# Performance work log

Measured on AMD Instinct MI355X. Metric: run time of the kernel, lower is better.

Reference implementation:

```python
import jax, jax.numpy as jnp
import numpy as np

EPS = 1e-5
SLOPE = 0.2

def _leaky(x):
    return jnp.where(x >= 0, x, SLOPE * x)

def _bn(x, g, b, axes):
    # batch-norm in training mode: biased stats over `axes`, per remaining channel dim
    mu = jnp.mean(x, axis=axes, keepdims=True)
    var = jnp.var(x, axis=axes, keepdims=True)
    shape = [1] * x.ndim
    shape[2 if x.ndim == 5 else 1] = -1
    return (x - mu) * jax.lax.rsqrt(var + EPS) * g.reshape(shape) + b.reshape(shape)

def setup_inputs() -> dict:
    key = jax.random.key(0)
    ks = jax.random.split(key, 6)
    T, B, C, H, W, D = 17, 16, 512, 16, 16, 256
    return {
        "cond": jax.random.normal(ks[0], (B, D), jnp.float32),
        "xbar": jax.random.normal(ks[1], (T, B, C, H, W), jnp.float32),
        "lin_w": jax.random.normal(ks[2], (D, D), jnp.float32) * 0.05,
        "lin_b": jnp.zeros((D,), jnp.float32),
        "bn_s_g": jnp.ones((D,), jnp.float32),
        "bn_s_b": jnp.zeros((D,), jnp.float32),
        "conv1_w": jax.random.normal(ks[3], (C, C), jnp.float32) * 0.05,
        "bn1_g": jnp.ones((C,), jnp.float32),
        "bn1_b": jnp.zeros((C,), jnp.float32),
        "conv2_w": jax.random.normal(ks[4], (C, C + D), jnp.float32) * 0.05,
        "bn2_g": jnp.ones((C,), jnp.float32),
        "bn2_b": jnp.zeros((C,), jnp.float32),
        "conv3_w": jax.random.normal(ks[5], (1, C, 2, 2), jnp.float32) * 0.05,
    }

def reference(cond, xbar, lin_w, lin_b, bn_s_g, bn_s_b, conv1_w, bn1_g, bn1_b, conv2_w, bn2_g, bn2_b, conv3_w):
    # sent_map: Linear -> BatchNorm1d (over batch) -> LeakyReLU
    sent = cond @ lin_w.T + lin_b                       # [B, D]
    sent = _leaky(_bn(sent, bn_s_g, bn_s_b, axes=(0,)))

    motions = xbar[1:] - xbar[:-1]                      # [F, B, C, H, W]
    F, B, C, H, W = motions.shape

    # motion_map: 1x1 conv -> BN (per-frame stats, matching the python loop) -> LeakyReLU
    h = jnp.einsum('fbchw,oc->fbohw', motions, conv1_w)
    h = _leaky(_bn(h, bn1_g, bn1_b, axes=(1, 3, 4)))

    # broadcast sentence vector over space (replaces per-pixel python loop)
    sent_dupe = jnp.broadcast_to(sent[None, :, :, None, None], (F, B, sent.shape[1], H, W))
    ms = jnp.concatenate([h, sent_dupe], axis=2)        # [F, B, C+D, H, W]

    # predictor: 1x1 conv -> BN (per-frame) -> LeakyReLU -> 2x2 stride-2 conv
    h2 = jnp.einsum('fbchw,oc->fbohw', ms, conv2_w)
    h2 = _leaky(_bn(h2, bn2_g, bn2_b, axes=(1, 3, 4)))

    h2f = h2.reshape(F * B, C, H, W)
    out = jax.lax.conv_general_dilated(
        h2f, conv3_w, window_strides=(2, 2), padding='VALID',
        dimension_numbers=('NCHW', 'OIHW', 'NCHW'))     # [F*B, 1, H/2, W/2]
    return out.reshape(F, B, -1)                        # matches view(B,-1) per frame + stack
```

## Files before the change

### kernel.cpp

```cpp
#include <hip/hip_runtime.h>
#include <hip/hip_bf16.h>

#define EPS 1e-5f
#define SLOPE 0.2f

#define NF 16
#define NBATCH 16
#define NC 512
#define NHW 256
#define ND 256
#define K2 768
#define MF 4096
#define FRAME_ELEMS ((size_t)MF * NC)

typedef __attribute__((ext_vector_type(8))) short short8;
typedef __attribute__((ext_vector_type(4))) float float4v;

__device__ __forceinline__ float lrelu(float v) { return v >= 0.f ? v : SLOPE * v; }
__device__ __forceinline__ float b2f(ushort u) { union { float f; uint i; } x; x.i = ((uint)u) << 16; return x.f; }
__device__ __forceinline__ ushort f2b(float f) {
  uint i = __float_as_uint(f);
  return (ushort)((i + 0x7FFFu + ((i >> 16) & 1u)) >> 16);
}
__device__ __forceinline__ void gl16(const ushort* g, ushort* l) {
  __builtin_amdgcn_global_load_lds(
      (const __attribute__((address_space(1))) unsigned int*)g,
      (__attribute__((address_space(3))) unsigned int*)l, 16, 0, 0);
}

__global__ __launch_bounds__(256) void k_sent(
    const float* __restrict__ cond, const float* __restrict__ lin_w,
    const float* __restrict__ lin_b, const float* __restrict__ gam,
    const float* __restrict__ bet, float* __restrict__ sent) {
  int d = threadIdx.x;
  float acc[NBATCH];
  float bias = lin_b[d];
#pragma unroll
  for (int b = 0; b < NBATCH; ++b) acc[b] = bias;
  for (int k = 0; k < ND; ++k) {
    float w = lin_w[d * ND + k];
#pragma unroll
    for (int b = 0; b < NBATCH; ++b) acc[b] = fmaf(cond[b * ND + k], w, acc[b]);
  }
  float mu = 0.f;
#pragma unroll
  for (int b = 0; b < NBATCH; ++b) mu += acc[b];
  mu *= (1.f / NBATCH);
  float var = 0.f;
#pragma unroll
  for (int b = 0; b < NBATCH; ++b) { float t = acc[b] - mu; var = fmaf(t, t, var); }
  var *= (1.f / NBATCH);
  float sc = rsqrtf(var + EPS) * gam[d];
  float sh = bet[d] - mu * sc;
#pragma unroll
  for (int b = 0; b < NBATCH; ++b) sent[b * ND + d] = lrelu(fmaf(acc[b], sc, sh));
}

__global__ __launch_bounds__(256) void k_bias2(
    const float* __restrict__ sent, const float* __restrict__ w2,
    float* __restrict__ bias2) {
  int o = blockIdx.x * 256 + threadIdx.x;
  float acc[NBATCH];
#pragma unroll
  for (int b = 0; b < NBATCH; ++b) acc[b] = 0.f;
  for (int d = 0; d < ND; ++d) {
    float w = w2[(size_t)o * K2 + NC + d];
#pragma unroll
    for (int b = 0; b < NBATCH; ++b) acc[b] = fmaf(sent[b * ND + d], w, acc[b]);
  }
#pragma unroll
  for (int b = 0; b < NBATCH; ++b) bias2[b * NC + o] = acc[b];
}

__global__ __launch_bounds__(256) void k_wcvt(
    const float* __restrict__ w1, const float* __restrict__ w2,
    ushort* __restrict__ w1b, ushort* __restrict__ w2b) {
  int i = blockIdx.x * 256 + threadIdx.x;
  w1b[i] = f2b(w1[i]);
  int o = i >> 9, c = i & 511;
  w2b[i] = f2b(w2[(size_t)o * K2 + c]);
}

__global__ __launch_bounds__(256) void k_mot(
    const float* __restrict__ xbar, ushort* __restrict__ mot, int f0, int nb) {
  __shared__ float T[64][65];
  int b = blockIdx.y;
  int hw0 = (blockIdx.x & 3) * 64;
  int c0 = (blockIdx.x >> 2) * 64;
  int t = threadIdx.x;
  int w = t >> 6, l = t & 63;
  int fs = blockIdx.z * 4;
  int fe = fs + 4 < nb ? fs + 4 : nb;

  const float* xp = xbar + ((size_t)(f0 + fs) * NBATCH + b) * (NC * NHW) + hw0 + l;
  float prev[16];
#pragma unroll
  for (int k = 0; k < 16; ++k) prev[k] = xp[(size_t)(c0 + 4 * k + w) * NHW];

  for (int fr = fs; fr < fe; ++fr) {
    const float* xc = xbar + ((size_t)(f0 + fr + 1) * NBATCH + b) * (NC * NHW) + hw0 + l;
    float cur[16];
#pragma unroll
    for (int k = 0; k < 16; ++k) cur[k] = xc[(size_t)(c0 + 4 * k + w) * NHW];
#pragma unroll
    for (int k = 0; k < 16; ++k) T[4 * k + w][l] = cur[k] - prev[k];
    __syncthreads();
    ushort* mp = mot + ((size_t)fr * MF + b * NHW + hw0) * NC + c0;
#pragma unroll
    for (int k = 0; k < 16; ++k) mp[(size_t)(4 * k + w) * NC + l] = f2b(T[l][4 * k + w]);
    __syncthreads();
#pragma unroll
    for (int k = 0; k < 16; ++k) prev[k] = cur[k];
  }
}

template <int BIAS>
__global__ __launch_bounds__(256) void k_gemm(
    const ushort* __restrict__ A, const ushort* __restrict__ W,
    const float* __restrict__ bias2, ushort* __restrict__ H,
    float2* __restrict__ part) {
  __shared__ ushort lds[2][8192];
  int t = threadIdx.x;
  int w = t >> 6, l = t & 63;
  int g = blockIdx.z;
  int m0 = blockIdx.x * 128;
  int n0 = blockIdx.y * 128;
  int wr = w >> 1, wc = w & 1;

  const ushort* Ag = A + ((size_t)g * MF + m0) * NC;
  const ushort* Wg = W + (size_t)n0 * NC;

  float4v acc[4][4];
#pragma unroll
  for (int i = 0; i < 4; ++i)
#pragma unroll
    for (int j = 0; j < 4; ++j) acc[i][j] = (float4v)0.f;

  int s1 = (w * 2 + 0) * 64 + l;
  int s2 = (w * 2 + 1) * 64 + l;
  size_t ga1 = (size_t)(s1 >> 2) * NC + (s1 & 3) * 8;
  size_t ga2 = (size_t)(s2 >> 2) * NC + (s2 & 3) * 8;

#define STAGE(buf, c0)                                  \
  do {                                                  \
    gl16(Ag + ga1 + (c0), &lds[buf][s1 * 8]);           \
    gl16(Ag + ga2 + (c0), &lds[buf][s2 * 8]);           \
    gl16(Wg + ga1 + (c0), &lds[buf][4096 + s1 * 8]);    \
    gl16(Wg + ga2 + (c0), &lds[buf][4096 + s2 * 8]);    \
  } while (0)

  STAGE(0, 0);
  asm volatile("s_waitcnt vmcnt(0)" ::: "memory");
  __syncthreads();

  for (int kt = 0; kt < 16; ++kt) {
    int cur = kt & 1;
    if (kt < 15) STAGE(cur ^ 1, (kt + 1) * 32);
    short8 af[4], bfr[4];
#pragma unroll
    for (int i = 0; i < 4; ++i)
      af[i] = *(const short8*)&lds[cur][(wr * 64 + i * 16 + (l & 15)) * 32 + (l >> 4) * 8];
#pragma unroll
    for (int j = 0; j < 4; ++j)
      bfr[j] = *(const short8*)&lds[cur][4096 + (wc * 64 + j * 16 + (l & 15)) * 32 + (l >> 4) * 8];
#pragma unroll
    for (int i = 0; i < 4; ++i)
#pragma unroll
      for (int j = 0; j < 4; ++j)
        acc[i][j] = __builtin_amdgcn_mfma_f32_16x16x32_bf16(af[i], bfr[j], acc[i][j], 0, 0, 0);
    if (kt < 15) {
      asm volatile("s_waitcnt vmcnt(0)" ::: "memory");
      __syncthreads();
    }
  }
#undef STAGE
  __syncthreads();

  float bz[4];
#pragma unroll
  for (int fn = 0; fn < 4; ++fn)
    bz[fn] = BIAS ? bias2[(m0 >> 8) * NC + n0 + wc * 64 + fn * 16 + (l & 15)] : 0.f;

  float sv[4], qv[4];
#pragma unroll
  for (int fn = 0; fn < 4; ++fn) {
    float s = 0.f, q = 0.f;
#pragma unroll
    for (int fm = 0; fm < 4; ++fm)
#pragma unroll
      for (int j = 0; j < 4; ++j) {
        float v = acc[fm][fn][j] + bz[fn];
        acc[fm][fn][j] = v;
        s += v;
        q = fmaf(v, v, q);
      }
    s += __shfl_xor(s, 16); s += __shfl_xor(s, 32);
    q += __shfl_xor(q, 16); q += __shfl_xor(q, 32);
    sv[fn] = s; qv[fn] = q;
  }
  if (l < 16) {
    int mb = blockIdx.x * 2 + wr;
    float2* pp = part + ((size_t)g * 64 + mb) * NC + n0 + wc * 64 + l;
#pragma unroll
    for (int fn = 0; fn < 4; ++fn) pp[fn * 16] = make_float2(sv[fn], qv[fn]);
  }

  ushort* ep = &lds[0][w * 1088];
  ushort* Hg = H + ((size_t)g * MF + m0 + wr * 64) * NC + n0 + wc * 64;
#pragma unroll
  for (int fm = 0; fm < 4; ++fm) {
#pragma unroll
    for (int fn = 0; fn < 4; ++fn)
#pragma unroll
      for (int j = 0; j < 4; ++j)
        ep[((l >> 4) * 4 + j) * 68 + fn * 16 + (l & 15)] = f2b(acc[fm][fn][j]);
#pragma unroll
    for (int h = 0; h < 2; ++h) {
      int r = h * 8 + (l >> 3), sl = l & 7;
      short8 v = *(const short8*)&ep[r * 68 + sl * 8];
      *(short8*)&Hg[(size_t)(fm * 16 + r) * NC + sl * 8] = v;
    }
  }
}

__global__ __launch_bounds__(256) void k_stats2(
    const float2* __restrict__ part, const float* __restrict__ gam,
    const float* __restrict__ bet, float2* __restrict__ st) {
  int bi = blockIdx.x;
  int g = bi >> 1;
  int o = (bi & 1) * 256 + threadIdx.x;
  float s = 0.f, q = 0.f;
#pragma unroll
  for (int mb = 0; mb < 64; ++mb) {
    float2 v = part[((size_t)g * 64 + mb) * NC + o];
    s += v.x;
    q += v.y;
  }
  float mu = s * (1.f / 4096.f);
  float var = q * (1.f / 4096.f) - mu * mu;
  float sc = rsqrtf(var + EPS) * gam[o];
  st[g * NC + o] = make_float2(sc, bet[o] - mu * sc);
}

__global__ __launch_bounds__(256) void k_act(
    const ushort* __restrict__ h1, const float2* __restrict__ st,
    ushort* __restrict__ a2) {
  int g = blockIdx.z;
  size_t i0 = ((size_t)blockIdx.x * 256 + threadIdx.x) * 8;
  int o0 = (int)(i0 & 511);
  const ushort* src = h1 + (size_t)g * FRAME_ELEMS + i0;
  ushort* dst = a2 + (size_t)g * FRAME_ELEMS + i0;
  short8 v = *(const short8*)src;
  short8 r;
#pragma unroll
  for (int e = 0; e < 8; ++e) {
    float2 ss = st[g * NC + o0 + e];
    float x = fmaf(b2f((ushort)v[e]), ss.x, ss.y);
    r[e] = (short)f2b(lrelu(x));
  }
  *(short8*)dst = r;
}

__global__ __launch_bounds__(256) void k_conv3(
    const ushort* __restrict__ h2, const float2* __restrict__ st2,
    const float* __restrict__ w3, float* __restrict__ out, int f0) {
  int g = blockIdx.z;
  int b = blockIdx.x;
  int t = threadIdx.x;
  int oi = t >> 2;
  int cs = t & 3;
  int y = oi >> 3, x = oi & 7;
  const ushort* base = h2 + ((size_t)g * MF + b * NHW) * NC;
  int m00 = (2 * y) * 16 + 2 * x;
  float acc = 0.f;
  for (int c8 = cs * 128; c8 < cs * 128 + 128; c8 += 8) {
    short8 v0 = *(const short8*)&base[(size_t)(m00 + 0) * NC + c8];
    short8 v1 = *(const short8*)&base[(size_t)(m00 + 1) * NC + c8];
    short8 v2 = *(const short8*)&base[(size_t)(m00 + 16) * NC + c8];
    short8 v3 = *(const short8*)&base[(size_t)(m00 + 17) * NC + c8];
#pragma unroll
    for (int e = 0; e < 8; ++e) {
      float2 ss = st2[g * NC + c8 + e];
      float4 wv = ((const float4*)w3)[c8 + e];
      acc = fmaf(lrelu(fmaf(b2f((ushort)v0[e]), ss.x, ss.y)), wv.x, acc);
      acc = fmaf(lrelu(fmaf(b2f((ushort)v1[e]), ss.x, ss.y)), wv.y, acc);
      acc = fmaf(lrelu(fmaf(b2f((ushort)v2[e]), ss.x, ss.y)), wv.z, acc);
      acc = fmaf(lrelu(fmaf(b2f((ushort)v3[e]), ss.x, ss.y)), wv.w, acc);
    }
  }
  acc += __shfl_xor(acc, 1);
  acc += __shfl_xor(acc, 2);
  if (cs == 0) out[((size_t)(f0 + g) * NBATCH + b) * 64 + oi] = acc;
}

extern "C" void kernel_launch(void* const* d_in, const int* in_sizes, int n_in,
                              void* d_out, int out_size, void* d_ws, size_t ws_size,
                              hipStream_t stream) {
  const float* cond = (const float*)d_in[0];
  const float* xbar = (const float*)d_in[1];
  const float* lin_w = (const float*)d_in[2];
  const float* lin_b = (const float*)d_in[3];
  const float* bnsg = (const float*)d_in[4];
  const float* bnsb = (const float*)d_in[5];
  const float* w1 = (const float*)d_in[6];
  const float* bn1g = (const float*)d_in[7];
  const float* bn1b = (const float*)d_in[8];
  const float* w2 = (const float*)d_in[9];
  const float* bn2g = (const float*)d_in[10];
  const float* bn2b = (const float*)d_in[11];
  const float* w3 = (const float*)d_in[12];
  float* out = (float*)d_out;

  char* p = (char*)d_ws;
  float* sent = (float*)p;    p += ((NBATCH * ND * 4 + 255) & ~255);
  float* bias2 = (float*)p;   p += ((NBATCH * NC * 4 + 255) & ~255);
  float2* st1 = (float2*)p;   p += ((NF * NC * 8 + 255) & ~255);
  float2* st2 = (float2*)p;   p += ((NF * NC * 8 + 255) & ~255);
  float2* part = (float2*)p;  p += (((size_t)NF * 64 * NC * 8 + 255) & ~255);
  ushort* w1b = (ushort*)p;   p += ((NC * NC * 2 + 255) & ~255);
  ushort* w2b = (ushort*)p;   p += ((NC * NC * 2 + 255) & ~255);
  size_t used = (size_t)(p - (char*)d_ws);
  const size_t frame_bytes = FRAME_ELEMS * 2;
  size_t rem = ws_size > used ? ws_size - used : 0;
  int FB = (int)(rem / (3 * frame_bytes));
  if (FB < 1) FB = 1;
  if (FB > NF) FB = NF;
  ushort* bufA = (ushort*)p;
  ushort* bufB = bufA + (size_t)FB * FRAME_ELEMS;
  ushort* bufC = bufB + (size_t)FB * FRAME_ELEMS;

  k_wcvt<<<1024, 256, 0, stream>>>(w1, w2, w1b, w2b);
  k_sent<<<1, 256, 0, stream>>>(cond, lin_w, lin_b, bnsg, bnsb, sent);
  k_bias2<<<2, 256, 0, stream>>>(sent, w2, bias2);

  for (int f0 = 0; f0 < NF; f0 += FB) {
    int nb = (NF - f0) < FB ? (NF - f0) : FB;
    int ngrp = (nb + 3) / 4;
    k_mot<<<dim3(32, NBATCH, ngrp), 256, 0, stream>>>(xbar, bufA, f0, nb);
    k_gemm<0><<<dim3(32, 4, nb), 256, 0, stream>>>(bufA, w1b, nullptr, bufB, part);
    k_stats2<<<2 * nb, 256, 0, stream>>>(part, bn1g, bn1b, st1);
    k_act<<<dim3(1024, 1, nb), 256, 0, stream>>>(bufB, st1, bufA);
    k_gemm<1><<<dim3(32, 4, nb), 256, 0, stream>>>(bufA, w2b, bias2, bufC, part);
    k_stats2<<<2 * nb, 256, 0, stream>>>(part, bn2g, bn2b, st2);
    k_conv3<<<dim3(NBATCH, 1, nb), 256, 0, stream>>>(bufC, st2, w3, out, f0);
  }
}
```

Before: 306.4 us.

## Fuse BN1 activation into second GEMM prologue and rework GEMM pipelining with swizzled LDS

Removes the standalone k_act pass. The second GEMM now loads raw conv1 outputs through registers, applies the BN scale/shift and LeakyReLU, and writes the result into LDS, which saves a full read and write of the activation buffer. Both GEMMs get an XOR-swizzled LDS layout to cut bank conflicts, a two-stage-ahead prefetch with partial vmcnt waits, a fully unrolled K loop, and launch_bounds occupancy 2. Smaller changes spread k_sent over 4 blocks and have k_mot handle 8 frames per block. The trade-off is more VALU work and register pressure inside the GEMM main loop.

```diff
diff --git a/kernel.cpp b/kernel.cpp
--- a/kernel.cpp
+++ b/kernel.cpp
@@ -28,11 +28,11 @@
       (__attribute__((address_space(3))) unsigned int*)l, 16, 0, 0);
 }
 
-__global__ __launch_bounds__(256) void k_sent(
+__global__ __launch_bounds__(64) void k_sent(
     const float* __restrict__ cond, const float* __restrict__ lin_w,
     const float* __restrict__ lin_b, const float* __restrict__ gam,
     const float* __restrict__ bet, float* __restrict__ sent) {
-  int d = threadIdx.x;
+  int d = blockIdx.x * 64 + threadIdx.x;
   float acc[NBATCH];
   float bias = lin_b[d];
 #pragma unroll
@@ -89,8 +89,8 @@
   int c0 = (blockIdx.x >> 2) * 64;
   int t = threadIdx.x;
   int w = t >> 6, l = t & 63;
-  int fs = blockIdx.z * 4;
-  int fe = fs + 4 < nb ? fs + 4 : nb;
+  int fs = blockIdx.z * 8;
+  int fe = fs + 8 < nb ? fs + 8 : nb;
 
   const float* xp = xbar + ((size_t)(f0 + fs) * NBATCH + b) * (NC * NHW) + hw0 + l;
   float prev[16];
@@ -114,72 +114,14 @@
   }
 }
 
-template <int BIAS>
-__global__ __launch_bounds__(256) void k_gemm(
-    const ushort* __restrict__ A, const ushort* __restrict__ W,
-    const float* __restrict__ bias2, ushort* __restrict__ H,
-    float2* __restrict__ part) {
-  __shared__ ushort lds[2][8192];
-  int t = threadIdx.x;
-  int w = t >> 6, l = t & 63;
-  int g = blockIdx.z;
-  int m0 = blockIdx.x * 128;
-  int n0 = blockIdx.y * 128;
-  int wr = w >> 1, wc = w & 1;
-
-  const ushort* Ag = A + ((size_t)g * MF + m0) * NC;
-  const ushort* Wg = W + (size_t)n0 * NC;
-
-  float4v acc[4][4];
-#pragma unroll
-  for (int i = 0; i < 4; ++i)
-#pragma unroll
-    for (int j = 0; j < 4; ++j) acc[i][j] = (float4v)0.f;
-
-  int s1 = (w * 2 + 0) * 64 + l;
-  int s2 = (w * 2 + 1) * 64 + l;
-  size_t ga1 = (size_t)(s1 >> 2) * NC + (s1 & 3) * 8;
-  size_t ga2 = (size_t)(s2 >> 2) * NC + (s2 & 3) * 8;
-
-#define STAGE(buf, c0)                                  \
-  do {                                                  \
-    gl16(Ag + ga1 + (c0), &lds[buf][s1 * 8]);           \
-    gl16(Ag + ga2 + (c0), &lds[buf][s2 * 8]);           \
-    gl16(Wg + ga1 + (c0), &lds[buf][4096 + s1 * 8]);    \
-    gl16(Wg + ga2 + (c0), &lds[buf][4096 + s2 * 8]);    \
-  } while (0)
-
-  STAGE(0, 0);
-  asm volatile("s_waitcnt vmcnt(0)" ::: "memory");
-  __syncthreads();
-
-  for (int kt = 0; kt < 16; ++kt) {
-    int cur = kt & 1;
-    if (kt < 15) STAGE(cur ^ 1, (kt + 1) * 32);
-    short8 af[4], bfr[4];
-#pragma unroll
-    for (int i = 0; i < 4; ++i)
-      af[i] = *(const short8*)&lds[cur][(wr * 64 + i * 16 + (l & 15)) * 32 + (l >> 4) * 8];
-#pragma unroll
-    for (int j = 0; j < 4; ++j)
-      bfr[j] = *(const short8*)&lds[cur][4096 + (wc * 64 + j * 16 + (l & 15)) * 32 + (l >> 4) * 8];
-#pragma unroll
-    for (int i = 0; i < 4; ++i)
-#pragma unroll
-      for (int j = 0; j < 4; ++j)
-        acc[i][j] = __builtin_amdgcn_mfma_f32_16x16x32_bf16(af[i], bfr[j], acc[i][j], 0, 0, 0);
-    if (kt < 15) {
-      asm volatile("s_waitcnt vmcnt(0)" ::: "memory");
-      __syncthreads();
-    }
-  }
-#undef STAGE
-  __syncthreads();
-
+__device__ __forceinline__ void gemm_epilogue(
+    float4v (&acc)[4][4], ushort* lds0, const float* bias2, int has_bias,
+    ushort* __restrict__ H, float2* __restrict__ part,
+    int g, int m0, int n0, int w, int l, int wr, int wc) {
   float bz[4];
 #pragma unroll
   for (int fn = 0; fn < 4; ++fn)
-    bz[fn] = BIAS ? bias2[(m0 >> 8) * NC + n0 + wc * 64 + fn * 16 + (l & 15)] : 0.f;
+    bz[fn] = has_bias ? bias2[(m0 >> 8) * NC + n0 + wc * 64 + fn * 16 + (l & 15)] : 0.f;
 
   float sv[4], qv[4];
 #pragma unroll
@@ -199,13 +141,13 @@
     sv[fn] = s; qv[fn] = q;
   }
   if (l < 16) {
-    int mb = blockIdx.x * 2 + wr;
+    int mb = (m0 >> 6) + wr;
     float2* pp = part + ((size_t)g * 64 + mb) * NC + n0 + wc * 64 + l;
 #pragma unroll
     for (int fn = 0; fn < 4; ++fn) pp[fn * 16] = make_float2(sv[fn], qv[fn]);
   }
 
-  ushort* ep = &lds[0][w * 1088];
+  ushort* ep = &lds0[w * 1088];
   ushort* Hg = H + ((size_t)g * MF + m0 + wr * 64) * NC + n0 + wc * 64;
 #pragma unroll
   for (int fm = 0; fm < 4; ++fm) {
@@ -221,6 +163,202 @@
       *(short8*)&Hg[(size_t)(fm * 16 + r) * NC + sl * 8] = v;
     }
   }
+}
+
+__global__ __launch_bounds__(256, 2) void k_gemm1(
+    const ushort* __restrict__ A, const ushort* __restrict__ W,
+    ushort* __restrict__ H, float2* __restrict__ part) {
+  __shared__ ushort lds[2][8192];
+  int t = threadIdx.x, w = t >> 6, l = t & 63;
+  int g = blockIdx.z, m0 = blockIdx.x * 128, n0 = blockIdx.y * 128;
+  int wr = w >> 1, wc = w & 1;
+  const ushort* Ag = A + ((size_t)g * MF + m0) * NC;
+  const ushort* Wg = W + (size_t)n0 * NC;
+  int s1 = w * 128 + l, s2 = s1 + 64;
+  size_t ga1 = (size_t)(s1 >> 2) * NC + (((s1 & 3) ^ ((s1 >> 3) & 3)) * 8);
+  size_t ga2 = (size_t)(s2 >> 2) * NC + (((s2 & 3) ^ ((s2 >> 3) & 3)) * 8);
+
+#define STAGE1(buf, c0)                               \
+  do {                                                \
+    gl16(Ag + ga1 + (c0), &lds[buf][s1 * 8]);         \
+    gl16(Ag + ga2 + (c0), &lds[buf][s2 * 8]);         \
+    gl16(Wg + ga1 + (c0), &lds[buf][4096 + s1 * 8]);  \
+    gl16(Wg + ga2 + (c0), &lds[buf][4096 + s2 * 8]);  \
+  } while (0)
+
+  STAGE1(0, 0);
+  STAGE1(1, 32);
+
+  float4v acc[4][4];
+#pragma unroll
+  for (int i = 0; i < 4; ++i)
+#pragma unroll
+    for (int j = 0; j < 4; ++j) acc[i][j] = (float4v)0.f;
+
+  int xr = ((l & 15) >> 1) & 3;
+  int co = ((l >> 4) ^ xr) * 8;
+  int aoff[4], boff[4];
+#pragma unroll
+  for (int i = 0; i < 4; ++i) aoff[i] = (wr * 64 + i * 16 + (l & 15)) * 32 + co;
+#pragma unroll
+  for (int j = 0; j < 4; ++j) boff[j] = 4096 + (wc * 64 + j * 16 + (l & 15)) * 32 + co;
+
+  asm volatile("s_waitcnt vmcnt(0)" ::: "memory");
+  __builtin_amdgcn_sched_barrier(0);
+  __builtin_amdgcn_s_barrier();
+  __builtin_amdgcn_sched_barrier(0);
+
+#pragma unroll
+  for (int kt = 0; kt < 16; ++kt) {
+    const int cur = kt & 1;
+    short8 af[4], bfr[4];
+#pragma unroll
+    for (int i = 0; i < 4; ++i) af[i] = *(const short8*)&lds[cur][aoff[i]];
+#pragma unroll
+    for (int j = 0; j < 4; ++j) bfr[j] = *(const short8*)&lds[cur][boff[j]];
+    asm volatile("s_waitcnt lgkmcnt(0)" ::: "memory");
+    __builtin_amdgcn_sched_barrier(0);
+    __builtin_amdgcn_s_barrier();
+    __builtin_amdgcn_sched_barrier(0);
+    if (kt < 14) STAGE1(cur, (kt + 2) * 32);
+#pragma unroll
+    for (int i = 0; i < 4; ++i)
+#pragma unroll
+      for (int j = 0; j < 4; ++j)
+        acc[i][j] = __builtin_amdgcn_mfma_f32_16x16x32_bf16(af[i], bfr[j], acc[i][j], 0, 0, 0);
+    if (kt < 15) {
+      if (kt < 14) asm volatile("s_waitcnt vmcnt(4)" ::: "memory");
+      else         asm volatile("s_waitcnt vmcnt(0)" ::: "memory");
+      __builtin_amdgcn_sched_barrier(0);
+      __builtin_amdgcn_s_barrier();
+      __builtin_amdgcn_sched_barrier(0);
+    }
+  }
+#undef STAGE1
+  gemm_epilogue(acc, &lds[0][0], nullptr, 0, H, part, g, m0, n0, w, l, wr, wc);
+}
+
+__global__ __launch_bounds__(256, 2) void k_gemm2(
+    const ushort* __restrict__ A, const ushort* __restrict__ W,
+    const float2* __restrict__ st, const float* __restrict__ bias2,
+    ushort* __restrict__ H, float2* __restrict__ part) {
+  __shared__ ushort lds[2][8192];
+  __shared__ float2 stl[NC];
+  int t = threadIdx.x, w = t >> 6, l = t & 63;
+  int g = blockIdx.z, m0 = blockIdx.x * 128, n0 = blockIdx.y * 128;
+  int wr = w >> 1, wc = w & 1;
+  const ushort* Ag = A + ((size_t)g * MF + m0) * NC;
+  const ushort* Wg = W + (size_t)n0 * NC;
+  int s1 = w * 128 + l, s2 = s1 + 64;
+  int kb1 = (s1 & 3) ^ ((s1 >> 3) & 3);
+  int kb2 = (s2 & 3) ^ ((s2 >> 3) & 3);
+  size_t gb1 = (size_t)(s1 >> 2) * NC + kb1 * 8;
+  size_t gb2 = (size_t)(s2 >> 2) * NC + kb2 * 8;
+  const ushort* As1 = Ag + gb1;
+  const ushort* As2 = Ag + gb2;
+
+#define XFORM(aV, sr, dst)                              \
+  do {                                                  \
+    uint outw[4];                                       \
+    _Pragma("unroll") for (int q = 0; q < 4; ++q) {     \
+      uint u = ((const uint*)&(aV))[q];                 \
+      float f0 = __uint_as_float(u << 16);              \
+      float f1 = __uint_as_float(u & 0xffff0000u);      \
+      float x0 = fmaf(f0, sr[2 * q].x, sr[2 * q].y);    \
+      float x1 = fmaf(f1, sr[2 * q + 1].x, sr[2 * q + 1].y); \
+      x0 = fmaxf(x0, SLOPE * x0);                       \
+      x1 = fmaxf(x1, SLOPE * x1);                       \
+      outw[q] = ((uint)f2b(x1) << 16) | (uint)f2b(x0);  \
+    }                                                   \
+    *(uint4*)(dst) = *(const uint4*)outw;               \
+  } while (0)
+
+  uint4 asA[2], asB[2];
+  gl16((const ushort*)(st + (size_t)g * NC) + t * 8, (ushort*)stl + t * 8);
+  gl16(Wg + gb1 + 0, &lds[0][4096 + s1 * 8]);
+  gl16(Wg + gb2 + 0, &lds[0][4096 + s2 * 8]);
+  gl16(Wg + gb1 + 32, &lds[1][4096 + s1 * 8]);
+  gl16(Wg + gb2 + 32, &lds[1][4096 + s2 * 8]);
+  uint4 t0A = *(const uint4*)(As1);
+  uint4 t0B = *(const uint4*)(As2);
+  asA[1] = *(const uint4*)(As1 + 32);
+  asB[1] = *(const uint4*)(As2 + 32);
+
+  float4v acc[4][4];
+#pragma unroll
+  for (int i = 0; i < 4; ++i)
+#pragma unroll
+    for (int j = 0; j < 4; ++j) acc[i][j] = (float4v)0.f;
+
+  int xr = ((l & 15) >> 1) & 3;
+  int co = ((l >> 4) ^ xr) * 8;
+  int aoff[4], boff[4];
+#pragma unroll
+  for (int i = 0; i < 4; ++i) aoff[i] = (wr * 64 + i * 16 + (l & 15)) * 32 + co;
+#pragma unroll
+  for (int j = 0; j < 4; ++j) boff[j] = 4096 + (wc * 64 + j * 16 + (l & 15)) * 32 + co;
+
+  asm volatile("s_waitcnt vmcnt(0)" ::: "memory");
+  __builtin_amdgcn_sched_barrier(0);
+  __builtin_amdgcn_s_barrier();
+  __builtin_amdgcn_sched_barrier(0);
+  {
+    float2 sr1[8], sr2[8];
+#pragma unroll
+    for (int e = 0; e < 8; ++e) { sr1[e] = stl[kb1 * 8 + e]; sr2[e] = stl[kb2 * 8 + e]; }
+    XFORM(t0A, sr1, &lds[0][s1 * 8]);
+    XFORM(t0B, sr2, &lds[0][s2 * 8]);
+  }
+  asm volatile("s_waitcnt lgkmcnt(0)" ::: "memory");
+  __builtin_amdgcn_sched_barrier(0);
+  __builtin_amdgcn_s_barrier();
+  __builtin_amdgcn_sched_barrier(0);
+
+#pragma unroll
+  for (int kt = 0; kt < 16; ++kt) {
+    const int cur = kt & 1;
+    short8 af[4], bfr[4];
+#pragma unroll
+    for (int i = 0; i < 4; ++i) af[i] = *(const short8*)&lds[cur][aoff[i]];
+#pragma unroll
+    for (int j = 0; j < 4; ++j) bfr[j] = *(const short8*)&lds[cur][boff[j]];
+    float2 sr1[8], sr2[8];
+    if (kt < 15) {
+      int k01 = (kt + 1) * 32 + kb1 * 8;
+      int k02 = (kt + 1) * 32 + kb2 * 8;
+#pragma unroll
+      for (int e = 0; e < 8; ++e) { sr1[e] = stl[k01 + e]; sr2[e] = stl[k02 + e]; }
+    }
+    asm volatile("s_waitcnt lgkmcnt(0)" ::: "memory");
+    __builtin_amdgcn_sched_barrier(0);
+    __builtin_amdgcn_s_barrier();
+    __builtin_amdgcn_sched_barrier(0);
+    if (kt < 14) {
+      int c2 = (kt + 2) * 32;
+      asA[kt & 1] = *(const uint4*)(As1 + c2);
+      asB[kt & 1] = *(const uint4*)(As2 + c2);
+      gl16(Wg + gb1 + c2, &lds[cur][4096 + s1 * 8]);
+      gl16(Wg + gb2 + c2, &lds[cur][4096 + s2 * 8]);
+    }
+#pragma unroll
+    for (int i = 0; i < 4; ++i)
+#pragma unroll
+      for (int j = 0; j < 4; ++j)
+        acc[i][j] = __builtin_amdgcn_mfma_f32_16x16x32_bf16(af[i], bfr[j], acc[i][j], 0, 0, 0);
+    if (kt < 15) {
+      if (kt < 14) asm volatile("s_waitcnt vmcnt(4)" ::: "memory");
+      else         asm volatile("s_waitcnt vmcnt(0)" ::: "memory");
+      __builtin_amdgcn_sched_barrier(0);
+      XFORM(asA[(kt + 1) & 1], sr1, &lds[cur ^ 1][s1 * 8]);
+      XFORM(asB[(kt + 1) & 1], sr2, &lds[cur ^ 1][s2 * 8]);
+      asm volatile("s_waitcnt lgkmcnt(0)" ::: "memory");
+      __builtin_amdgcn_sched_barrier(0);
+      __builtin_amdgcn_s_barrier();
+      __builtin_amdgcn_sched_barrier(0);
+    }
+  }
+#undef XFORM
+  gemm_epilogue(acc, &lds[0][0], bias2, 1, H, part, g, m0, n0, w, l, wr, wc);
 }
 
 __global__ __launch_bounds__(256) void k_stats2(
@@ -240,25 +378,6 @@
   float var = q * (1.f / 4096.f) - mu * mu;
   float sc = rsqrtf(var + EPS) * gam[o];
   st[g * NC + o] = make_float2(sc, bet[o] - mu * sc);
-}
-
-__global__ __launch_bounds__(256) void k_act(
-    const ushort* __restrict__ h1, const float2* __restrict__ st,
-    ushort* __restrict__ a2) {
-  int g = blockIdx.z;
-  size_t i0 = ((size_t)blockIdx.x * 256 + threadIdx.x) * 8;
-  int o0 = (int)(i0 & 511);
-  const ushort* src = h1 + (size_t)g * FRAME_ELEMS + i0;
-  ushort* dst = a2 + (size_t)g * FRAME_ELEMS + i0;
-  short8 v = *(const short8*)src;
-  short8 r;
-#pragma unroll
-  for (int e = 0; e < 8; ++e) {
-    float2 ss = st[g * NC + o0 + e];
-    float x = fmaf(b2f((ushort)v[e]), ss.x, ss.y);
-    r[e] = (short)f2b(lrelu(x));
-  }
-  *(short8*)dst = r;
 }
 
 __global__ __launch_bounds__(256) void k_conv3(
@@ -330,17 +449,16 @@
   ushort* bufC = bufB + (size_t)FB * FRAME_ELEMS;
 
   k_wcvt<<<1024, 256, 0, stream>>>(w1, w2, w1b, w2b);
-  k_sent<<<1, 256, 0, stream>>>(cond, lin_w, lin_b, bnsg, bnsb, sent);
+  k_sent<<<4, 64, 0, stream>>>(cond, lin_w, lin_b, bnsg, bnsb, sent);
   k_bias2<<<2, 256, 0, stream>>>(sent, w2, bias2);
 
   for (int f0 = 0; f0 < NF; f0 += FB) {
     int nb = (NF - f0) < FB ? (NF - f0) : FB;
-    int ngrp = (nb + 3) / 4;
+    int ngrp = (nb + 7) / 8;
     k_mot<<<dim3(32, NBATCH, ngrp), 256, 0, stream>>>(xbar, bufA, f0, nb);
-    k_gemm<0><<<dim3(32, 4, nb), 256, 0, stream>>>(bufA, w1b, nullptr, bufB, part);
+    k_gemm1<<<dim3(32, 4, nb), 256, 0, stream>>>(bufA, w1b, bufB, part);
     k_stats2<<<2 * nb, 256, 0, stream>>>(part, bn1g, bn1b, st1);
-    k_act<<<dim3(1024, 1, nb), 256, 0, stream>>>(bufB, st1, bufA);
-    k_gemm<1><<<dim3(32, 4, nb), 256, 0, stream>>>(bufA, w2b, bias2, bufC, part);
+    k_gemm2<<<dim3(32, 4, nb), 256, 0, stream>>>(bufB, w2b, st1, bias2, bufC, part);
     k_stats2<<<2 * nb, 256, 0, stream>>>(part, bn2g, bn2b, st2);
     k_conv3<<<dim3(NBATCH, 1, nb), 256, 0, stream>>>(bufC, st2, w3, out, f0);
   }
```

Result: faster. 279.0 us (-8.9%).
